# Kernel optimization log

Measured on AMD Instinct MI355X. Metric: run time of the kernel, lower is better.

Reference implementation:

```python
import jax, jax.numpy as jnp
import numpy as np

B, N, XDIM, EDIM, H = 4, 256, 256, 128, 8
DF = XDIM // H


def _linear_params(key, din, dout):
    k1, k2 = jax.random.split(key)
    s = 1.0 / np.sqrt(din)
    W = jax.random.uniform(k1, (din, dout), minval=-s, maxval=s, dtype=jnp.float32)
    b = jax.random.uniform(k2, (dout,), minval=-s, maxval=s, dtype=jnp.float32)
    return W, b


def setup_inputs() -> dict:
    key = jax.random.key(0)
    ks = jax.random.split(key, 9)
    x = jax.random.normal(ks[0], (B, N, XDIM), dtype=jnp.float32)
    e = jax.random.normal(ks[1], (B, N, N, EDIM), dtype=jnp.float32)
    Wq, bq = _linear_params(ks[2], XDIM, XDIM)
    Wk, bk = _linear_params(ks[3], XDIM, XDIM)
    Wv, bv = _linear_params(ks[4], XDIM, XDIM)
    Wem, bem = _linear_params(ks[5], EDIM, XDIM)  # e_mul
    Wea, bea = _linear_params(ks[6], EDIM, XDIM)  # e_add
    Wxo, bxo = _linear_params(ks[7], XDIM, XDIM)  # x_out
    Weo, beo = _linear_params(ks[8], XDIM, EDIM)  # e_out
    return {"x": x, "e": e, "Wq": Wq, "bq": bq, "Wk": Wk, "bk": bk,
            "Wv": Wv, "bv": bv, "Wem": Wem, "bem": bem, "Wea": Wea, "bea": bea,
            "Wxo": Wxo, "bxo": bxo, "Weo": Weo, "beo": beo}


def reference(x, e, Wq, bq, Wk, bk, Wv, bv, Wem, bem, Wea, bea, Wxo, bxo, Weo, beo):
    Bq, Nq, _ = x.shape
    # per-node projections -> [B, N, H, DF]
    Q = (x @ Wq + bq).reshape(Bq, Nq, H, DF)
    K = (x @ Wk + bk).reshape(Bq, Nq, H, DF)
    V = (x @ Wv + bv).reshape(Bq, Nq, H, DF)
    # broadcasted outer product: Y[b,i,j,h,d] = Q[b,i,h,d] * K[b,j,h,d] / sqrt(DF)
    Y = Q[:, :, None] * K[:, None] * (1.0 / np.sqrt(DF))  # [B,N,N,H,DF]
    # edge modulation
    E1 = (e @ Wem + bem).reshape(Bq, Nq, Nq, H, DF)
    E2 = (e @ Wea + bea).reshape(Bq, Nq, Nq, H, DF)
    Y = Y * (E1 + 1.0) + E2
    # new edge features
    newE = Y.reshape(Bq, Nq, Nq, XDIM) @ Weo + beo  # [B,N,N,EDIM]
    # attention: softmax over the FIRST node axis (dim=1), as in the torch code
    attn = jax.nn.softmax(Y, axis=1)  # [B,N,N,H,DF]
    # weighted_V[b,j,h,d] = sum_i attn[b,i,j,h,d] * V[b,j,h,d]
    weighted_V = jnp.sum(attn * V[:, None], axis=1)  # [B,N,H,DF]
    newX = weighted_V.reshape(Bq, Nq, XDIM) @ Wxo + bxo  # [B,N,XDIM]
    return (newX, newE)
```

## Files before the change

### kernel.cpp

```cpp
#include <hip/hip_runtime.h>

#define NN 256
#define XD 256
#define ED 128

typedef __attribute__((ext_vector_type(8))) short short8;
typedef __attribute__((ext_vector_type(4))) float f32x4;

__device__ __forceinline__ unsigned short f2bf(float f) {
    unsigned u = __builtin_bit_cast(unsigned, f);
    u += 0x7FFF + ((u >> 16) & 1);
    return (unsigned short)(u >> 16);
}

#define MFMA16(a, b, c) __builtin_amdgcn_mfma_f32_16x16x32_bf16(a, b, c, 0, 0, 0)

__global__ __launch_bounds__(256) void wprep_kernel(
    const float* __restrict__ Wq, const float* __restrict__ Wk,
    const float* __restrict__ Wv, const float* __restrict__ Wxo,
    const float* __restrict__ Wem, const float* __restrict__ Wea,
    const float* __restrict__ Weo,
    short* __restrict__ WqT, short* __restrict__ WkT,
    short* __restrict__ WvT, short* __restrict__ WxoT,
    short* __restrict__ WemT, short* __restrict__ WeaT,
    short* __restrict__ WeoT)
{
    __shared__ float sT[32][33];
    int blk = blockIdx.x;
    const float* src; short* dst; int din, dout, tile;
    if (blk < 256) {
        int m = blk >> 6; tile = blk & 63; din = 256; dout = 256;
        src = m == 0 ? Wq : (m == 1 ? Wk : (m == 2 ? Wv : Wxo));
        dst = m == 0 ? WqT : (m == 1 ? WkT : (m == 2 ? WvT : WxoT));
    } else if (blk < 320) {
        int m = (blk - 256) >> 5; tile = (blk - 256) & 31; din = 128; dout = 256;
        src = m == 0 ? Wem : Wea; dst = m == 0 ? WemT : WeaT;
    } else {
        tile = blk - 320; din = 256; dout = 128;
        src = Weo; dst = WeoT;
    }
    int ksh = (din == 256) ? 3 : 2;
    int kt = tile & ((1 << ksh) - 1);
    int nt = tile >> ksh;
    int c = threadIdx.x & 31, rbase = threadIdx.x >> 5;
    #pragma unroll
    for (int p = 0; p < 4; ++p) {
        int r = rbase + p * 8;
        sT[r][c] = src[(kt * 32 + r) * dout + nt * 32 + c];
    }
    __syncthreads();
    #pragma unroll
    for (int p = 0; p < 4; ++p) {
        int r = rbase + p * 8;
        dst[(nt * 32 + r) * din + kt * 32 + c] = (short)f2bf(sT[c][r]);
    }
}

__global__ __launch_bounds__(512) void proj_qk_kernel(
    const float* __restrict__ x, const short* __restrict__ WqT,
    const short* __restrict__ WkT, const float* __restrict__ bq,
    const float* __restrict__ bk, float* __restrict__ Qs,
    float* __restrict__ KT)
{
    __shared__ unsigned short sX[64 * 264];
    const int blk = blockIdx.x;
    const int mtile = blk >> 1;
    const int mat   = blk & 1;
    const int tid = threadIdx.x, wave = tid >> 6, lane = tid & 63;
    const int quad = lane >> 4, l16 = lane & 15;

    {
        const float4* src4 = (const float4*)(x + (size_t)mtile * 64 * XD);
        #pragma unroll
        for (int it = 0; it < 8; ++it) {
            int idx4 = tid + it * 512;
            float4 v = src4[idx4];
            int elem = idx4 * 4, row = elem >> 8, col = elem & 255;
            short4 p = make_short4((short)f2bf(v.x), (short)f2bf(v.y),
                                   (short)f2bf(v.z), (short)f2bf(v.w));
            *(short4*)&sX[row * 264 + col] = p;
        }
    }
    __syncthreads();

    const short* WT   = mat ? WkT : WqT;
    const float* bias = mat ? bk : bq;
    const int c0 = wave * 32;

    f32x4 acc[4][2] = {};
    for (int ks = 0; ks < 8; ++ks) {
        short8 bfrag[2];
        #pragma unroll
        for (int ct = 0; ct < 2; ++ct)
            bfrag[ct] = *(const short8*)&WT[(c0 + ct * 16 + l16) * 256 + ks * 32 + quad * 8];
        #pragma unroll
        for (int mt = 0; mt < 4; ++mt) {
            short8 a = *(const short8*)&sX[(mt * 16 + l16) * 264 + ks * 32 + quad * 8];
            acc[mt][0] = MFMA16(a, bfrag[0], acc[mt][0]);
            acc[mt][1] = MFMA16(a, bfrag[1], acc[mt][1]);
        }
    }

    if (mat == 0) {
        #pragma unroll
        for (int mt = 0; mt < 4; ++mt)
            #pragma unroll
            for (int ct = 0; ct < 2; ++ct) {
                int cc = c0 + ct * 16 + l16;
                float bb = bias[cc];
                #pragma unroll
                for (int r = 0; r < 4; ++r)
                    Qs[(size_t)(mtile * 64 + mt * 16 + quad * 4 + r) * 256 + cc] =
                        (acc[mt][ct][r] + bb) * 0.17677669529663687f;
            }
    } else {
        int b = mtile >> 2, j0p = (mtile & 3) * 64;
        #pragma unroll
        for (int mt = 0; mt < 4; ++mt)
            #pragma unroll
            for (int ct = 0; ct < 2; ++ct) {
                int cc = c0 + ct * 16 + l16;
                float bb = bias[cc];
                f32x4 st;
                #pragma unroll
                for (int r = 0; r < 4; ++r) st[r] = acc[mt][ct][r] + bb;
                *(f32x4*)&KT[(size_t)(b * 256 + cc) * 256 + j0p + mt * 16 + quad * 4] = st;
            }
    }
}

__global__ __launch_bounds__(512) void proj_vx_kernel(
    const float* __restrict__ x, const short* __restrict__ WvT,
    const float* __restrict__ bv, const short* __restrict__ WxoT,
    const float* __restrict__ bxo, float* __restrict__ outX)
{
    __shared__ unsigned short sX[64 * 264];
    __shared__ unsigned short sV[64 * 264];
    const int mtile = blockIdx.x;
    const int tid = threadIdx.x, wave = tid >> 6, lane = tid & 63;
    const int quad = lane >> 4, l16 = lane & 15;

    {
        const float4* src4 = (const float4*)(x + (size_t)mtile * 64 * XD);
        #pragma unroll
        for (int it = 0; it < 8; ++it) {
            int idx4 = tid + it * 512;
            float4 v = src4[idx4];
            int elem = idx4 * 4, row = elem >> 8, col = elem & 255;
            short4 p = make_short4((short)f2bf(v.x), (short)f2bf(v.y),
                                   (short)f2bf(v.z), (short)f2bf(v.w));
            *(short4*)&sX[row * 264 + col] = p;
        }
    }
    __syncthreads();

    const int c0 = wave * 32;
    f32x4 acc[4][2] = {};
    for (int ks = 0; ks < 8; ++ks) {
        short8 bfrag[2];
        #pragma unroll
        for (int ct = 0; ct < 2; ++ct)
            bfrag[ct] = *(const short8*)&WvT[(c0 + ct * 16 + l16) * 256 + ks * 32 + quad * 8];
        #pragma unroll
        for (int mt = 0; mt < 4; ++mt) {
            short8 a = *(const short8*)&sX[(mt * 16 + l16) * 264 + ks * 32 + quad * 8];
            acc[mt][0] = MFMA16(a, bfrag[0], acc[mt][0]);
            acc[mt][1] = MFMA16(a, bfrag[1], acc[mt][1]);
        }
    }
    #pragma unroll
    for (int mt = 0; mt < 4; ++mt)
        #pragma unroll
        for (int ct = 0; ct < 2; ++ct) {
            int cc = c0 + ct * 16 + l16;
            float bb = bv[cc];
            #pragma unroll
            for (int r = 0; r < 4; ++r)
                sV[(mt * 16 + quad * 4 + r) * 264 + cc] = f2bf(acc[mt][ct][r] + bb);
        }
    __syncthreads();

    f32x4 acc2[4][2] = {};
    for (int ks = 0; ks < 8; ++ks) {
        short8 bfrag[2];
        #pragma unroll
        for (int ct = 0; ct < 2; ++ct)
            bfrag[ct] = *(const short8*)&WxoT[(c0 + ct * 16 + l16) * 256 + ks * 32 + quad * 8];
        #pragma unroll
        for (int mt = 0; mt < 4; ++mt) {
            short8 a = *(const short8*)&sV[(mt * 16 + l16) * 264 + ks * 32 + quad * 8];
            acc2[mt][0] = MFMA16(a, bfrag[0], acc2[mt][0]);
            acc2[mt][1] = MFMA16(a, bfrag[1], acc2[mt][1]);
        }
    }
    #pragma unroll
    for (int mt = 0; mt < 4; ++mt)
        #pragma unroll
        for (int ct = 0; ct < 2; ++ct) {
            int cc = c0 + ct * 16 + l16;
            float bb = bxo[cc];
            #pragma unroll
            for (int r = 0; r < 4; ++r)
                outX[(size_t)(mtile * 64 + mt * 16 + quad * 4 + r) * 256 + cc] =
                    acc2[mt][ct][r] + bb;
        }
}

__global__ __launch_bounds__(256, 3) void fused_edge_kernel(
    const float* __restrict__ e, const float* __restrict__ Qs,
    const float* __restrict__ KT, const short* __restrict__ WemT,
    const short* __restrict__ WeaT, const short* __restrict__ WeoT,
    const float* __restrict__ bem, const float* __restrict__ bea,
    const float* __restrict__ beo, float* __restrict__ outE)
{
    __shared__ unsigned short sE[64 * 140];
    __shared__ unsigned short sY[64 * 268];

    const int blk  = blockIdx.x;
    const int jq   = blk & 3;
    const int i    = (blk >> 2) & 255;
    const int b    = blk >> 10;
    const int j0   = jq * 64;
    const int tid  = threadIdx.x;
    const int wave = tid >> 6;
    const int lane = tid & 63;
    const int quad = lane >> 4;
    const int l16  = lane & 15;

    {
        const f32x4* src4 = (const f32x4*)(e + (size_t)((b * NN + i) * NN + j0) * ED);
        #pragma unroll
        for (int it = 0; it < 8; ++it) {
            int idx4 = tid + it * 256;
            f32x4 v = __builtin_nontemporal_load(&src4[idx4]);
            int elem = idx4 * 4, row = elem >> 7, col = elem & 127;
            short4 p = make_short4((short)f2bf(v[0]), (short)f2bf(v[1]),
                                   (short)f2bf(v[2]), (short)f2bf(v[3]));
            *(short4*)&sE[row * 140 + col] = p;
        }
    }

    const float* Qrow = Qs + (size_t)(b * NN + i) * XD;
    float bo[2];
    #pragma unroll
    for (int ct = 0; ct < 2; ++ct) bo[ct] = beo[wave * 32 + ct * 16 + l16];

    __syncthreads();

    #pragma unroll
    for (int p = 0; p < 2; ++p) {
        const int c0 = wave * 32 + p * 128;
        float qsv[2], bmv[2], bav[2];
        int ktA[2];
        #pragma unroll
        for (int ct = 0; ct < 2; ++ct) {
            int cc = c0 + ct * 16 + l16;
            qsv[ct] = Qrow[cc];
            bmv[ct] = bem[cc] + 1.0f;
            bav[ct] = bea[cc];
            ktA[ct] = (b * 256 + cc) * 256 + j0 + quad * 4;
        }
        short8 B1[4][2], B2[4][2];
        #pragma unroll
        for (int ks = 0; ks < 4; ++ks)
            #pragma unroll
            for (int ct = 0; ct < 2; ++ct) {
                int n = c0 + ct * 16 + l16;
                B1[ks][ct] = *(const short8*)&WemT[n * 128 + ks * 32 + quad * 8];
                B2[ks][ct] = *(const short8*)&WeaT[n * 128 + ks * 32 + quad * 8];
            }
        f32x4 kvp[4][2];
        #pragma unroll
        for (int mc = 0; mc < 4; ++mc)
            #pragma unroll
            for (int ct = 0; ct < 2; ++ct)
                kvp[mc][ct] = *(const f32x4*)&KT[ktA[ct] + mc * 16];
        #pragma unroll
        for (int mc = 0; mc < 4; ++mc) {
            const int m0 = mc * 16;
            f32x4 aE1[2] = {}, aE2[2] = {};
            __builtin_amdgcn_s_setprio(1);
            #pragma unroll
            for (int ks = 0; ks < 4; ++ks) {
                short8 a = *(const short8*)&sE[(m0 + l16) * 140 + ks * 32 + quad * 8];
                aE1[0] = MFMA16(a, B1[ks][0], aE1[0]);
                aE1[1] = MFMA16(a, B1[ks][1], aE1[1]);
                aE2[0] = MFMA16(a, B2[ks][0], aE2[0]);
                aE2[1] = MFMA16(a, B2[ks][1], aE2[1]);
            }
            __builtin_amdgcn_s_setprio(0);
            #pragma unroll
            for (int ct = 0; ct < 2; ++ct) {
                int cc = c0 + ct * 16 + l16;
                #pragma unroll
                for (int r = 0; r < 4; ++r) {
                    float y = qsv[ct] * kvp[mc][ct][r] * (aE1[ct][r] + bmv[ct])
                              + (aE2[ct][r] + bav[ct]);
                    sY[(m0 + quad * 4 + r) * 268 + cc] = f2bf(y);
                }
            }
        }
    }

    short8 B3[8][2];
    #pragma unroll
    for (int ks = 0; ks < 8; ++ks)
        #pragma unroll
        for (int ct = 0; ct < 2; ++ct)
            B3[ks][ct] = *(const short8*)&WeoT[(wave * 32 + ct * 16 + l16) * 256 + ks * 32 + quad * 8];
    __syncthreads();

    f32x4 acc2[4][2] = {};
    __builtin_amdgcn_s_setprio(1);
    #pragma unroll
    for (int ks = 0; ks < 8; ++ks) {
        #pragma unroll
        for (int mt = 0; mt < 4; ++mt) {
            short8 a = *(const short8*)&sY[(mt * 16 + l16) * 268 + ks * 32 + quad * 8];
            acc2[mt][0] = MFMA16(a, B3[ks][0], acc2[mt][0]);
            acc2[mt][1] = MFMA16(a, B3[ks][1], acc2[mt][1]);
        }
    }
    __builtin_amdgcn_s_setprio(0);
    float* outBase = outE + (size_t)((b * NN + i) * NN + j0) * ED;
    #pragma unroll
    for (int mt = 0; mt < 4; ++mt)
        #pragma unroll
        for (int ct = 0; ct < 2; ++ct) {
            int col = wave * 32 + ct * 16 + l16;
            #pragma unroll
            for (int r = 0; r < 4; ++r)
                __builtin_nontemporal_store(acc2[mt][ct][r] + bo[ct],
                    &outBase[(size_t)(mt * 16 + quad * 4 + r) * ED + col]);
        }
}

extern "C" void kernel_launch(void* const* d_in, const int* in_sizes, int n_in,
                              void* d_out, int out_size, void* d_ws, size_t ws_size,
                              hipStream_t stream)
{
    const float* x   = (const float*)d_in[0];
    const float* e   = (const float*)d_in[1];
    const float* Wq  = (const float*)d_in[2];
    const float* bq  = (const float*)d_in[3];
    const float* Wk  = (const float*)d_in[4];
    const float* bk  = (const float*)d_in[5];
    const float* Wv  = (const float*)d_in[6];
    const float* bv  = (const float*)d_in[7];
    const float* Wem = (const float*)d_in[8];
    const float* bem = (const float*)d_in[9];
    const float* Wea = (const float*)d_in[10];
    const float* bea = (const float*)d_in[11];
    const float* Wxo = (const float*)d_in[12];
    const float* bxo = (const float*)d_in[13];
    const float* Weo = (const float*)d_in[14];
    const float* beo = (const float*)d_in[15];

    float* outX = (float*)d_out;
    float* outE = (float*)d_out + 262144;

    float* Qs   = (float*)d_ws;
    float* KT   = Qs + 262144;
    short* WqT  = (short*)(KT + 262144);
    short* WkT  = WqT + 65536;
    short* WvT  = WkT + 65536;
    short* WxoT = WvT + 65536;
    short* WemT = WxoT + 65536;
    short* WeaT = WemT + 32768;
    short* WeoT = WeaT + 32768;

    hipLaunchKernelGGL(wprep_kernel, dim3(352), dim3(256), 0, stream,
                       Wq, Wk, Wv, Wxo, Wem, Wea, Weo,
                       WqT, WkT, WvT, WxoT, WemT, WeaT, WeoT);
    hipLaunchKernelGGL(proj_qk_kernel, dim3(32), dim3(512), 0, stream,
                       x, WqT, WkT, bq, bk, Qs, KT);
    hipLaunchKernelGGL(proj_vx_kernel, dim3(16), dim3(512), 0, stream,
                       x, WvT, bv, WxoT, bxo, outX);
    hipLaunchKernelGGL(fused_edge_kernel, dim3(4096), dim3(256), 0, stream,
                       e, Qs, KT, WemT, WeaT, WeoT, bem, bea, beo, outE);
}
```

Measured before the change: 375.4 us.

## Swap MFMA operands in edge-output GEMM for vector stores, use packed bf16 convert

```diff
diff --git a/kernel.cpp b/kernel.cpp
--- a/kernel.cpp
+++ b/kernel.cpp
@@ -6,11 +6,18 @@
 
 typedef __attribute__((ext_vector_type(8))) short short8;
 typedef __attribute__((ext_vector_type(4))) float f32x4;
+typedef __attribute__((ext_vector_type(2))) unsigned int uint2v;
 
 __device__ __forceinline__ unsigned short f2bf(float f) {
     unsigned u = __builtin_bit_cast(unsigned, f);
     u += 0x7FFF + ((u >> 16) & 1);
     return (unsigned short)(u >> 16);
+}
+
+__device__ __forceinline__ unsigned cvtpk(float lo, float hi) {
+    unsigned r;
+    asm("v_cvt_pk_bf16_f32 %0, %1, %2" : "=v"(r) : "v"(lo), "v"(hi));
+    return r;
 }
 
 #define MFMA16(a, b, c) __builtin_amdgcn_mfma_f32_16x16x32_bf16(a, b, c, 0, 0, 0)
@@ -234,32 +241,38 @@
             int idx4 = tid + it * 256;
             f32x4 v = __builtin_nontemporal_load(&src4[idx4]);
             int elem = idx4 * 4, row = elem >> 7, col = elem & 127;
-            short4 p = make_short4((short)f2bf(v[0]), (short)f2bf(v[1]),
-                                   (short)f2bf(v[2]), (short)f2bf(v[3]));
-            *(short4*)&sE[row * 140 + col] = p;
+            uint2v p; p.x = cvtpk(v[0], v[1]); p.y = cvtpk(v[2], v[3]);
+            *(uint2v*)&sE[row * 140 + col] = p;
         }
     }
 
     const float* Qrow = Qs + (size_t)(b * NN + i) * XD;
-    float bo[2];
-    #pragma unroll
-    for (int ct = 0; ct < 2; ++ct) bo[ct] = beo[wave * 32 + ct * 16 + l16];
+    float qsv[2][2], bmv[2][2], bav[2][2];
+    int ktA[2][2];
+    #pragma unroll
+    for (int p = 0; p < 2; ++p)
+        #pragma unroll
+        for (int ct = 0; ct < 2; ++ct) {
+            int cc = wave * 32 + p * 128 + ct * 16 + l16;
+            qsv[p][ct] = Qrow[cc];
+            bmv[p][ct] = bem[cc] + 1.0f;
+            bav[p][ct] = bea[cc];
+            ktA[p][ct] = (b * 256 + cc) * 256 + j0 + quad * 4;
+        }
+    f32x4 kvp[2][4][2];
+    #pragma unroll
+    for (int p = 0; p < 2; ++p)
+        #pragma unroll
+        for (int mc = 0; mc < 4; ++mc)
+            #pragma unroll
+            for (int ct = 0; ct < 2; ++ct)
+                kvp[p][mc][ct] = *(const f32x4*)&KT[ktA[p][ct] + mc * 16];
 
     __syncthreads();
 
     #pragma unroll
     for (int p = 0; p < 2; ++p) {
         const int c0 = wave * 32 + p * 128;
-        float qsv[2], bmv[2], bav[2];
-        int ktA[2];
-        #pragma unroll
-        for (int ct = 0; ct < 2; ++ct) {
-            int cc = c0 + ct * 16 + l16;
-            qsv[ct] = Qrow[cc];
-            bmv[ct] = bem[cc] + 1.0f;
-            bav[ct] = bea[cc];
-            ktA[ct] = (b * 256 + cc) * 256 + j0 + quad * 4;
-        }
         short8 B1[4][2], B2[4][2];
         #pragma unroll
         for (int ks = 0; ks < 4; ++ks)
@@ -269,12 +282,6 @@
                 B1[ks][ct] = *(const short8*)&WemT[n * 128 + ks * 32 + quad * 8];
                 B2[ks][ct] = *(const short8*)&WeaT[n * 128 + ks * 32 + quad * 8];
             }
-        f32x4 kvp[4][2];
-        #pragma unroll
-        for (int mc = 0; mc < 4; ++mc)
-            #pragma unroll
-            for (int ct = 0; ct < 2; ++ct)
-                kvp[mc][ct] = *(const f32x4*)&KT[ktA[ct] + mc * 16];
         #pragma unroll
         for (int mc = 0; mc < 4; ++mc) {
             const int m0 = mc * 16;
@@ -292,47 +299,68 @@
             #pragma unroll
             for (int ct = 0; ct < 2; ++ct) {
                 int cc = c0 + ct * 16 + l16;
-                #pragma unroll
-                for (int r = 0; r < 4; ++r) {
-                    float y = qsv[ct] * kvp[mc][ct][r] * (aE1[ct][r] + bmv[ct])
-                              + (aE2[ct][r] + bav[ct]);
-                    sY[(m0 + quad * 4 + r) * 268 + cc] = f2bf(y);
-                }
+                float y0 = qsv[p][ct] * kvp[p][mc][ct][0] * (aE1[ct][0] + bmv[p][ct]) + (aE2[ct][0] + bav[p][ct]);
+                float y1 = qsv[p][ct] * kvp[p][mc][ct][1] * (aE1[ct][1] + bmv[p][ct]) + (aE2[ct][1] + bav[p][ct]);
+                float y2 = qsv[p][ct] * kvp[p][mc][ct][2] * (aE1[ct][2] + bmv[p][ct]) + (aE2[ct][2] + bav[p][ct]);
+                float y3 = qsv[p][ct] * kvp[p][mc][ct][3] * (aE1[ct][3] + bmv[p][ct]) + (aE2[ct][3] + bav[p][ct]);
+                unsigned u01 = cvtpk(y0, y1), u23 = cvtpk(y2, y3);
+                int rb = (m0 + quad * 4) * 268 + cc;
+                sY[rb]           = (unsigned short)u01;
+                sY[rb + 268]     = (unsigned short)(u01 >> 16);
+                sY[rb + 2 * 268] = (unsigned short)u23;
+                sY[rb + 3 * 268] = (unsigned short)(u23 >> 16);
             }
         }
     }
 
-    short8 B3[8][2];
-    #pragma unroll
-    for (int ks = 0; ks < 8; ++ks)
-        #pragma unroll
-        for (int ct = 0; ct < 2; ++ct)
-            B3[ks][ct] = *(const short8*)&WeoT[(wave * 32 + ct * 16 + l16) * 256 + ks * 32 + quad * 8];
-    __syncthreads();
-
-    f32x4 acc2[4][2] = {};
-    __builtin_amdgcn_s_setprio(1);
+    const int oH = (wave & 1) * 64;
+    const int jH = (wave >> 1) * 2;
+    short8 w01[2][4];
+    #pragma unroll
+    for (int ks = 0; ks < 2; ++ks)
+        #pragma unroll
+        for (int oT = 0; oT < 4; ++oT)
+            w01[ks][oT] = *(const short8*)&WeoT[(oH + oT * 16 + l16) * 256 + ks * 32 + quad * 8];
+    f32x4 bo4[4];
+    #pragma unroll
+    for (int oT = 0; oT < 4; ++oT)
+        bo4[oT] = *(const f32x4*)&beo[oH + oT * 16 + quad * 4];
+    __syncthreads();
+
+    f32x4 acc[4][2] = {};
     #pragma unroll
     for (int ks = 0; ks < 8; ++ks) {
-        #pragma unroll
-        for (int mt = 0; mt < 4; ++mt) {
-            short8 a = *(const short8*)&sY[(mt * 16 + l16) * 268 + ks * 32 + quad * 8];
-            acc2[mt][0] = MFMA16(a, B3[ks][0], acc2[mt][0]);
-            acc2[mt][1] = MFMA16(a, B3[ks][1], acc2[mt][1]);
-        }
-    }
-    __builtin_amdgcn_s_setprio(0);
+        short8 wo[4];
+        if (ks < 2) {
+            #pragma unroll
+            for (int oT = 0; oT < 4; ++oT) wo[oT] = w01[ks][oT];
+        } else {
+            #pragma unroll
+            for (int oT = 0; oT < 4; ++oT)
+                wo[oT] = *(const short8*)&WeoT[(oH + oT * 16 + l16) * 256 + ks * 32 + quad * 8];
+        }
+        __builtin_amdgcn_s_setprio(1);
+        #pragma unroll
+        for (int jt = 0; jt < 2; ++jt) {
+            short8 yb = *(const short8*)&sY[((jH + jt) * 16 + l16) * 268 + ks * 32 + quad * 8];
+            #pragma unroll
+            for (int oT = 0; oT < 4; ++oT)
+                acc[oT][jt] = MFMA16(wo[oT], yb, acc[oT][jt]);
+        }
+        __builtin_amdgcn_s_setprio(0);
+    }
+
     float* outBase = outE + (size_t)((b * NN + i) * NN + j0) * ED;
     #pragma unroll
-    for (int mt = 0; mt < 4; ++mt)
-        #pragma unroll
-        for (int ct = 0; ct < 2; ++ct) {
-            int col = wave * 32 + ct * 16 + l16;
-            #pragma unroll
-            for (int r = 0; r < 4; ++r)
-                __builtin_nontemporal_store(acc2[mt][ct][r] + bo[ct],
-                    &outBase[(size_t)(mt * 16 + quad * 4 + r) * ED + col]);
-        }
+    for (int oT = 0; oT < 4; ++oT) {
+        const int oq = oH + oT * 16 + quad * 4;
+        #pragma unroll
+        for (int jt = 0; jt < 2; ++jt) {
+            f32x4 st = acc[oT][jt] + bo4[oT];
+            __builtin_nontemporal_store(st,
+                (f32x4*)&outBase[(size_t)((jH + jt) * 16 + l16) * ED + oq]);
+        }
+    }
 }
 
 extern "C" void kernel_launch(void* const* d_in, const int* in_sizes, int n_in,
```

Result: slower. 409.9 us (+9.2%).
